# Performance work log

Hardware: AMD Instinct MI355X
Metric: run time of the kernel (lower is better)

## Reference

```python
import jax, jax.numpy as jnp
import numpy as np

B, N_ITEMS, H1, H2 = 1024, 50000, 600, 200


def setup_inputs() -> dict:
    key = jax.random.key(0)
    ks = jax.random.split(key, 8)
    return {
        "x": jax.random.uniform(ks[0], (B, N_ITEMS), dtype=jnp.float32),
        "W1": jax.random.normal(ks[1], (N_ITEMS, H1), dtype=jnp.float32) * 0.02,
        "b1": jax.random.normal(ks[2], (H1,), dtype=jnp.float32) * 0.001,
        "W2": jax.random.normal(ks[3], (H1, H2), dtype=jnp.float32) * 0.05,
        "b2": jax.random.normal(ks[4], (H2,), dtype=jnp.float32) * 0.001,
        "W3": jax.random.normal(ks[5], (H2, H1), dtype=jnp.float32) * 0.05,
        "b3": jax.random.normal(ks[6], (H1,), dtype=jnp.float32) * 0.001,
        "item_emb": jax.random.normal(ks[7], (N_ITEMS, H1), dtype=jnp.float32) * 0.02,
    }


def reference(x, W1, b1, W2, b2, W3, b3, item_emb):
    # F.normalize(input): L2-normalize rows with eps clamp
    norm = jnp.sqrt(jnp.sum(x * x, axis=-1, keepdims=True))
    h = x / jnp.maximum(norm, 1e-12)
    # tanh MLP stack (dropout is identity at inference)
    h = jnp.tanh(h @ W1 + b1)   # [B, 600]
    h = jnp.tanh(h @ W2 + b2)   # [B, 200]
    h = jnp.tanh(h @ W3 + b3)   # [B, 600]
    # pairwise squared-L2 distance to all item embeddings via GEMM decomposition:
    # ||h||^2 - 2 h.e + ||e||^2  (same math as the broadcasted (h-e)^2 sum)
    h_sq = jnp.sum(h * h, axis=-1, keepdims=True)          # [B, 1]
    e_sq = jnp.sum(item_emb * item_emb, axis=-1)           # [N]
    dist = h_sq - 2.0 * (h @ item_emb.T) + e_sq            # [B, N]
    return dist
```

## Files before the change

kernel.cpp:

```cpp
#include <hip/hip_runtime.h>
#include <stdint.h>

namespace {

constexpr int BROWS = 1024;
constexpr int NIT   = 50000;
constexpr int NH1   = 600;
constexpr int NH2   = 200;
constexpr int KXP   = 50016;
constexpr int N1P   = 640;
constexpr int NEP   = 50048;
constexpr int KEP   = 608;
constexpr int KI_TOTAL = KXP / 32;

typedef _Float16 f16x8 __attribute__((ext_vector_type(8)));
typedef _Float16 f16x4 __attribute__((ext_vector_type(4)));
typedef _Float16 f16x2 __attribute__((ext_vector_type(2)));
typedef float    f32x4 __attribute__((ext_vector_type(4)));

__device__ __forceinline__ void gld16(const void* g, void* l) {
  __builtin_amdgcn_global_load_lds(
      (__attribute__((address_space(1))) void*)(void*)g,
      (__attribute__((address_space(3))) void*)l, 16, 0, 0);
}

__global__ __launch_bounds__(256) void norm_conv_k(const float* __restrict__ x,
                                                   float* __restrict__ invnorm,
                                                   _Float16* __restrict__ xh) {
  const int row = blockIdx.x;
  const float4* xr = (const float4*)(x + (size_t)row * NIT);
  float ss = 0.f;
  if (xh != nullptr) {
    f16x4* xo = (f16x4*)(xh + (size_t)row * KXP);
    for (int i = threadIdx.x; i < NIT / 4; i += 256) {
      float4 v = xr[i];
      ss += v.x * v.x + v.y * v.y + v.z * v.z + v.w * v.w;
      f16x4 h;
      h.x = (_Float16)v.x; h.y = (_Float16)v.y;
      h.z = (_Float16)v.z; h.w = (_Float16)v.w;
      xo[i] = h;
    }
    if (threadIdx.x < (KXP - NIT) / 4) {
      f16x4 z;
      z.x = (_Float16)0.f; z.y = (_Float16)0.f;
      z.z = (_Float16)0.f; z.w = (_Float16)0.f;
      xo[NIT / 4 + threadIdx.x] = z;
    }
  } else {
    for (int i = threadIdx.x; i < NIT / 4; i += 256) {
      float4 v = xr[i];
      ss += v.x * v.x + v.y * v.y + v.z * v.z + v.w * v.w;
    }
  }
  for (int o = 32; o > 0; o >>= 1) ss += __shfl_down(ss, o);
  __shared__ float red[4];
  if ((threadIdx.x & 63) == 0) red[threadIdx.x >> 6] = ss;
  __syncthreads();
  if (threadIdx.x == 0) {
    float s = red[0] + red[1] + red[2] + red[3];
    invnorm[row] = 1.0f / fmaxf(sqrtf(s), 1e-12f);
  }
}

__global__ __launch_bounds__(256) void transpose_w1_k(const float* __restrict__ W1,
                                                      _Float16* __restrict__ W1T) {
  __shared__ float tile[64][65];
  const int kb = blockIdx.x * 64;
  const int nb = blockIdx.y * 64;
  const int t = threadIdx.x;
  #pragma unroll
  for (int i = 0; i < 16; ++i) {
    int idx = i * 256 + t;
    int k = idx >> 6, n = idx & 63;
    int gk = kb + k, gn = nb + n;
    tile[k][n] = (gk < NIT && gn < NH1) ? W1[(size_t)gk * NH1 + gn] : 0.f;
  }
  __syncthreads();
  #pragma unroll
  for (int i = 0; i < 8; ++i) {
    int idx = i * 256 + t;
    int n = idx >> 5;
    int k2 = (idx & 31) * 2;
    if (kb + k2 < KXP) {
      f16x2 h;
      h.x = (_Float16)tile[k2][n];
      h.y = (_Float16)tile[k2 + 1][n];
      *(f16x2*)(&W1T[(size_t)(nb + n) * KXP + kb + k2]) = h;
    }
  }
}

__global__ __launch_bounds__(256) void prep_emb_k(const float* __restrict__ emb,
                                                  _Float16* __restrict__ embb,
                                                  float* __restrict__ esq) {
  const int row = blockIdx.x * 4 + (threadIdx.x >> 6);
  const int lane = threadIdx.x & 63;
  const float* er = emb + (size_t)row * NH1;
  float ss = 0.f;
  #pragma unroll
  for (int j = 0; j < 10; ++j) {
    int idx = lane + 64 * j;
    float v = (row < NIT && idx < NH1) ? er[idx] : 0.f;
    ss += v * v;
    if (idx < KEP) embb[(size_t)row * KEP + idx] = (_Float16)v;
  }
  for (int o = 32; o > 0; o >>= 1) ss += __shfl_down(ss, o);
  if (lane == 0) esq[row] = ss;
}

template <int MODE>
__global__ __launch_bounds__(256) void mfma_nt_k(
    const void* __restrict__ Av, const _Float16* __restrict__ Bg,
    float* __restrict__ Cout, const float* __restrict__ hsq,
    const float* __restrict__ esq) {
  __shared__ _Float16 As[128 * 32];
  __shared__ _Float16 Bs[128 * 32];

  const int t = threadIdx.x;
  const int n0 = blockIdx.x * 128;
  const int m0 = blockIdx.y * 128;

  int ki0, ki1, lda, ldb;
  if (MODE == 1) {
    ki0 = 0; ki1 = KEP / 32; lda = KEP; ldb = KEP;
  } else {
    const int Z = (int)gridDim.z;
    const int kiPer = (KI_TOTAL + Z - 1) / Z;
    ki0 = blockIdx.z * kiPer;
    ki1 = ki0 + kiPer;
    if (ki1 > KI_TOTAL) ki1 = KI_TOTAL;
    lda = (MODE == 0) ? NIT : KXP;
    ldb = KXP;
  }

  const int lane = t & 63;
  const int wid = t >> 6;
  const int wm = wid >> 1, wn = wid & 1;
  const int lrow = lane & 15, quad = lane >> 4;

  const f32x4 zero = {0.f, 0.f, 0.f, 0.f};
  f32x4 acc[4][4];
  #pragma unroll
  for (int i = 0; i < 4; ++i)
    #pragma unroll
    for (int j = 0; j < 4; ++j) acc[i][j] = zero;

  for (int ki = ki0; ki < ki1; ++ki) {
    const int k0 = ki * 32;
    if (MODE == 0) {
      const float* A = (const float*)Av;
      #pragma unroll
      for (int j = 0; j < 4; ++j) {
        int g = j * 256 + t;
        int row = g >> 3;
        int kq = (g & 7) * 4;
        float4 v = {0.f, 0.f, 0.f, 0.f};
        if (k0 + kq < NIT)
          v = *(const float4*)(A + (size_t)(m0 + row) * lda + (k0 + kq));
        f16x4 h;
        h.x = (_Float16)v.x; h.y = (_Float16)v.y;
        h.z = (_Float16)v.z; h.w = (_Float16)v.w;
        *(f16x4*)(&As[row * 32 + kq]) = h;
      }
    } else {
      const _Float16* A = (const _Float16*)Av;
      #pragma unroll
      for (int j = 0; j < 2; ++j) {
        int c = j * 256 + t;
        int row = c >> 2, kk = (c & 3) * 8;
        gld16(A + (size_t)(m0 + row) * lda + (k0 + kk), &As[c * 8]);
      }
    }
    #pragma unroll
    for (int j = 0; j < 2; ++j) {
      int c = j * 256 + t;
      int row = c >> 2, kk = (c & 3) * 8;
      gld16(Bg + (size_t)(n0 + row) * ldb + (k0 + kk), &Bs[c * 8]);
    }
    __syncthreads();

    f16x8 af[4], bfr[4];
    #pragma unroll
    for (int mi = 0; mi < 4; ++mi)
      af[mi] = *(const f16x8*)(&As[(wm * 64 + mi * 16 + lrow) * 32 + quad * 8]);
    #pragma unroll
    for (int ni = 0; ni < 4; ++ni)
      bfr[ni] = *(const f16x8*)(&Bs[(wn * 64 + ni * 16 + lrow) * 32 + quad * 8]);
    #pragma unroll
    for (int mi = 0; mi < 4; ++mi)
      #pragma unroll
      for (int ni = 0; ni < 4; ++ni)
        acc[mi][ni] = __builtin_amdgcn_mfma_f32_16x16x32_f16(af[mi], bfr[ni],
                                                             acc[mi][ni], 0, 0, 0);
    __syncthreads();
  }

  if (MODE != 1) {
    float* Cs = Cout + (size_t)blockIdx.z * BROWS * N1P;
    #pragma unroll
    for (int mi = 0; mi < 4; ++mi)
      #pragma unroll
      for (int r = 0; r < 4; ++r) {
        int row = m0 + wm * 64 + mi * 16 + quad * 4 + r;
        #pragma unroll
        for (int ni = 0; ni < 4; ++ni) {
          int col = n0 + wn * 64 + ni * 16 + lrow;
          Cs[(size_t)row * N1P + col] = acc[mi][ni][r];
        }
      }
  } else {
    #pragma unroll
    for (int mi = 0; mi < 4; ++mi)
      #pragma unroll
      for (int r = 0; r < 4; ++r) {
        int row = m0 + wm * 64 + mi * 16 + quad * 4 + r;
        float hv = hsq[row];
        #pragma unroll
        for (int ni = 0; ni < 4; ++ni) {
          int col = n0 + wn * 64 + ni * 16 + lrow;
          if (col < NIT)
            Cout[(size_t)row * NIT + col] = hv - 2.f * acc[mi][ni][r] + esq[col];
        }
      }
  }
}

__global__ __launch_bounds__(256) void reduce_epi1_k(const float* __restrict__ C1p,
                                                     const float* __restrict__ invnorm,
                                                     const float* __restrict__ b1,
                                                     float* __restrict__ h1,
                                                     int nslabs) {
  int idx = blockIdx.x * 256 + threadIdx.x;
  if (idx >= BROWS * NH1) return;
  int m = idx / NH1, n = idx - m * NH1;
  float s = 0.f;
  for (int sp = 0; sp < nslabs; ++sp)
    s += C1p[(size_t)sp * BROWS * N1P + (size_t)m * N1P + n];
  h1[idx] = tanhf(invnorm[m] * s + b1[n]);
}

__global__ __launch_bounds__(256) void gemm2_k(const float* __restrict__ h1,
                                               const float* __restrict__ W2,
                                               const float* __restrict__ b2,
                                               float* __restrict__ h2) {
  __shared__ float hs[8 * NH1];
  const int m0 = blockIdx.x * 8;
  const int t = threadIdx.x;
  for (int i = t; i < 8 * NH1; i += 256) hs[i] = h1[(size_t)m0 * NH1 + i];
  __syncthreads();
  if (t < NH2) {
    float acc[8];
    #pragma unroll
    for (int r = 0; r < 8; ++r) acc[r] = 0.f;
    for (int k = 0; k < NH1; ++k) {
      float w = W2[k * NH2 + t];
      #pragma unroll
      for (int r = 0; r < 8; ++r) acc[r] += hs[r * NH1 + k] * w;
    }
    float bb = b2[t];
    #pragma unroll
    for (int r = 0; r < 8; ++r) h2[(size_t)(m0 + r) * NH2 + t] = tanhf(acc[r] + bb);
  }
}

__global__ __launch_bounds__(256) void gemm3_k(const float* __restrict__ h2,
                                               const float* __restrict__ W3,
                                               const float* __restrict__ b3,
                                               _Float16* __restrict__ h3h,
                                               float* __restrict__ hsq) {
  __shared__ float hs[8 * NH2];
  const int m0 = blockIdx.x * 8;
  const int t = threadIdx.x;
  for (int i = t; i < 8 * NH2; i += 256) hs[i] = h2[(size_t)m0 * NH2 + i];
  __syncthreads();
  float ssq[8];
  #pragma unroll
  for (int r = 0; r < 8; ++r) ssq[r] = 0.f;
  for (int c = 0; c < 3; ++c) {
    int n = t + c * 256;
    if (n < NH1) {
      float acc[8];
      #pragma unroll
      for (int r = 0; r < 8; ++r) acc[r] = 0.f;
      for (int k = 0; k < NH2; ++k) {
        float w = W3[k * NH1 + n];
        #pragma unroll
        for (int r = 0; r < 8; ++r) acc[r] += hs[r * NH2 + k] * w;
      }
      float bb = b3[n];
      #pragma unroll
      for (int r = 0; r < 8; ++r) {
        float v = tanhf(acc[r] + bb);
        h3h[(size_t)(m0 + r) * KEP + n] = (_Float16)v;
        ssq[r] += v * v;
      }
    } else if (n < KEP) {
      #pragma unroll
      for (int r = 0; r < 8; ++r) h3h[(size_t)(m0 + r) * KEP + n] = (_Float16)0.f;
    }
  }
  const int lane = t & 63, wid = t >> 6;
  #pragma unroll
  for (int r = 0; r < 8; ++r)
    for (int o = 32; o > 0; o >>= 1) ssq[r] += __shfl_down(ssq[r], o);
  __shared__ float red2[8][4];
  if (lane == 0) {
    #pragma unroll
    for (int r = 0; r < 8; ++r) red2[r][wid] = ssq[r];
  }
  __syncthreads();
  if (t < 8) hsq[m0 + t] = red2[t][0] + red2[t][1] + red2[t][2] + red2[t][3];
}

}

extern "C" void kernel_launch(void* const* d_in, const int* in_sizes, int n_in,
                              void* d_out, int out_size, void* d_ws, size_t ws_size,
                              hipStream_t stream) {
  const float* x   = (const float*)d_in[0];
  const float* W1  = (const float*)d_in[1];
  const float* b1  = (const float*)d_in[2];
  const float* W2  = (const float*)d_in[3];
  const float* b2  = (const float*)d_in[4];
  const float* W3  = (const float*)d_in[5];
  const float* b3  = (const float*)d_in[6];
  const float* emb = (const float*)d_in[7];
  float* out = (float*)d_out;

  char* ws = (char*)d_ws;

  const size_t XHSZ  = (size_t)BROWS * KXP * 2;
  const size_t W1TSZ = (size_t)N1P * KXP * 2;
  const size_t SLAB  = (size_t)BROWS * N1P * 4;
  const size_t TAIL  = 4096 + 200192 + 2457600 + 819200 + 1245184 + 4096;

  bool useF16A;
  int S;
  const size_t baseA = XHSZ + W1TSZ + TAIL;
  const size_t baseB = W1TSZ + TAIL;
  if (ws_size >= baseA + 16 * SLAB) {
    useF16A = true;
    size_t s = (ws_size - baseA) / SLAB;
    S = s > 32 ? 32 : (int)s;
  } else if (ws_size >= baseB + 8 * SLAB) {
    useF16A = false;
    size_t s = (ws_size - baseB) / SLAB;
    S = s > 32 ? 32 : (int)s;
  } else {
    return;
  }

  size_t off = 0;
  _Float16* xh = nullptr;
  if (useF16A) { xh = (_Float16*)(ws + off); off += XHSZ; }
  const size_t oW1T = off;
  _Float16* W1T = (_Float16*)(ws + off); off += W1TSZ;
  float* C1p = (float*)(ws + off); off += (size_t)S * SLAB;
  float* invn = (float*)(ws + off); off += 4096;
  float* esq  = (float*)(ws + off); off += 200192;
  float* h1   = (float*)(ws + off); off += 2457600;
  float* h2   = (float*)(ws + off); off += 819200;
  _Float16* h3h = (_Float16*)(ws + off); off += 1245184;
  float* hsq  = (float*)(ws + off); off += 4096;
  _Float16* embb = (_Float16*)(ws + oW1T);

  norm_conv_k<<<dim3(BROWS), dim3(256), 0, stream>>>(x, invn, xh);
  transpose_w1_k<<<dim3((KXP + 63) / 64, N1P / 64), dim3(256), 0, stream>>>(W1, W1T);
  if (useF16A) {
    mfma_nt_k<2><<<dim3(N1P / 128, BROWS / 128, S), dim3(256), 0, stream>>>(
        (const void*)xh, W1T, C1p, nullptr, nullptr);
  } else {
    mfma_nt_k<0><<<dim3(N1P / 128, BROWS / 128, S), dim3(256), 0, stream>>>(
        (const void*)x, W1T, C1p, nullptr, nullptr);
  }
  reduce_epi1_k<<<dim3((BROWS * NH1 + 255) / 256), dim3(256), 0, stream>>>(
      C1p, invn, b1, h1, S);
  prep_emb_k<<<dim3(NEP / 4), dim3(256), 0, stream>>>(emb, embb, esq);
  gemm2_k<<<dim3(BROWS / 8), dim3(256), 0, stream>>>(h1, W2, b2, h2);
  gemm3_k<<<dim3(BROWS / 8), dim3(256), 0, stream>>>(h2, W3, b3, h3h, hsq);
  mfma_nt_k<1><<<dim3(NEP / 128, BROWS / 128, 1), dim3(256), 0, stream>>>(
      (const void*)h3h, embb, out, hsq, esq);
}
```

Before: 1.036 ms.

## Double-buffer LDS tiles in MFMA GEMM and unroll the small GEMM loops

The MFMA GEMM kernel now keeps two LDS buffers. It issues the global-to-LDS loads for the next K tile before running the MFMAs on the current one, which hides load latency and needs only one barrier per iteration. An occupancy hint is added to the same kernel. The x row-norm loop is unrolled, and the small W2/W3 GEMMs batch 8 weight loads per step. KXP is padded to a multiple of 64 so the guard in the W1 transpose can be dropped. The cost is double the LDS use per block and larger padded buffers, which must still fit the workspace sizing.

New measurement: 1.010 ms. 1.03x faster.

```diff
diff --git a/kernel.cpp b/kernel.cpp
--- a/kernel.cpp
+++ b/kernel.cpp
@@ -7,7 +7,7 @@
 constexpr int NIT   = 50000;
 constexpr int NH1   = 600;
 constexpr int NH2   = 200;
-constexpr int KXP   = 50016;
+constexpr int KXP   = 50048;
 constexpr int N1P   = 640;
 constexpr int NEP   = 50048;
 constexpr int KEP   = 608;
@@ -32,6 +32,7 @@
   float ss = 0.f;
   if (xh != nullptr) {
     f16x4* xo = (f16x4*)(xh + (size_t)row * KXP);
+    #pragma unroll 4
     for (int i = threadIdx.x; i < NIT / 4; i += 256) {
       float4 v = xr[i];
       ss += v.x * v.x + v.y * v.y + v.z * v.z + v.w * v.w;
@@ -47,6 +48,7 @@
       xo[NIT / 4 + threadIdx.x] = z;
     }
   } else {
+    #pragma unroll 4
     for (int i = threadIdx.x; i < NIT / 4; i += 256) {
       float4 v = xr[i];
       ss += v.x * v.x + v.y * v.y + v.z * v.z + v.w * v.w;
@@ -81,12 +83,10 @@
     int idx = i * 256 + t;
     int n = idx >> 5;
     int k2 = (idx & 31) * 2;
-    if (kb + k2 < KXP) {
-      f16x2 h;
-      h.x = (_Float16)tile[k2][n];
-      h.y = (_Float16)tile[k2 + 1][n];
-      *(f16x2*)(&W1T[(size_t)(nb + n) * KXP + kb + k2]) = h;
-    }
+    f16x2 h;
+    h.x = (_Float16)tile[k2][n];
+    h.y = (_Float16)tile[k2 + 1][n];
+    *(f16x2*)(&W1T[(size_t)(nb + n) * KXP + kb + k2]) = h;
   }
 }
 
@@ -109,12 +109,12 @@
 }
 
 template <int MODE>
-__global__ __launch_bounds__(256) void mfma_nt_k(
+__global__ __launch_bounds__(256, 4) void mfma_nt_k(
     const void* __restrict__ Av, const _Float16* __restrict__ Bg,
     float* __restrict__ Cout, const float* __restrict__ hsq,
     const float* __restrict__ esq) {
-  __shared__ _Float16 As[128 * 32];
-  __shared__ _Float16 Bs[128 * 32];
+  __shared__ _Float16 As[2][128 * 32];
+  __shared__ _Float16 Bs[2][128 * 32];
 
   const int t = threadIdx.x;
   const int n0 = blockIdx.x * 128;
@@ -145,7 +145,7 @@
     #pragma unroll
     for (int j = 0; j < 4; ++j) acc[i][j] = zero;
 
-  for (int ki = ki0; ki < ki1; ++ki) {
+  auto stage = [&](int buf, int ki) {
     const int k0 = ki * 32;
     if (MODE == 0) {
       const float* A = (const float*)Av;
@@ -160,7 +160,7 @@
         f16x4 h;
         h.x = (_Float16)v.x; h.y = (_Float16)v.y;
         h.z = (_Float16)v.z; h.w = (_Float16)v.w;
-        *(f16x4*)(&As[row * 32 + kq]) = h;
+        *(f16x4*)(&As[buf][row * 32 + kq]) = h;
       }
     } else {
       const _Float16* A = (const _Float16*)Av;
@@ -168,24 +168,31 @@
       for (int j = 0; j < 2; ++j) {
         int c = j * 256 + t;
         int row = c >> 2, kk = (c & 3) * 8;
-        gld16(A + (size_t)(m0 + row) * lda + (k0 + kk), &As[c * 8]);
+        gld16(A + (size_t)(m0 + row) * lda + (k0 + kk), &As[buf][c * 8]);
       }
     }
     #pragma unroll
     for (int j = 0; j < 2; ++j) {
       int c = j * 256 + t;
       int row = c >> 2, kk = (c & 3) * 8;
-      gld16(Bg + (size_t)(n0 + row) * ldb + (k0 + kk), &Bs[c * 8]);
-    }
-    __syncthreads();
+      gld16(Bg + (size_t)(n0 + row) * ldb + (k0 + kk), &Bs[buf][c * 8]);
+    }
+  };
+
+  stage(0, ki0);
+  __syncthreads();
+
+  int cur = 0;
+  for (int ki = ki0; ki < ki1; ++ki) {
+    if (ki + 1 < ki1) stage(cur ^ 1, ki + 1);
 
     f16x8 af[4], bfr[4];
     #pragma unroll
     for (int mi = 0; mi < 4; ++mi)
-      af[mi] = *(const f16x8*)(&As[(wm * 64 + mi * 16 + lrow) * 32 + quad * 8]);
+      af[mi] = *(const f16x8*)(&As[cur][(wm * 64 + mi * 16 + lrow) * 32 + quad * 8]);
     #pragma unroll
     for (int ni = 0; ni < 4; ++ni)
-      bfr[ni] = *(const f16x8*)(&Bs[(wn * 64 + ni * 16 + lrow) * 32 + quad * 8]);
+      bfr[ni] = *(const f16x8*)(&Bs[cur][(wn * 64 + ni * 16 + lrow) * 32 + quad * 8]);
     #pragma unroll
     for (int mi = 0; mi < 4; ++mi)
       #pragma unroll
@@ -193,6 +200,7 @@
         acc[mi][ni] = __builtin_amdgcn_mfma_f32_16x16x32_f16(af[mi], bfr[ni],
                                                              acc[mi][ni], 0, 0, 0);
     __syncthreads();
+    cur ^= 1;
   }
 
   if (MODE != 1) {
@@ -252,10 +260,14 @@
     float acc[8];
     #pragma unroll
     for (int r = 0; r < 8; ++r) acc[r] = 0.f;
-    for (int k = 0; k < NH1; ++k) {
-      float w = W2[k * NH2 + t];
-      #pragma unroll
-      for (int r = 0; r < 8; ++r) acc[r] += hs[r * NH1 + k] * w;
+    for (int k0 = 0; k0 < NH1; k0 += 8) {
+      float w[8];
+      #pragma unroll
+      for (int u = 0; u < 8; ++u) w[u] = W2[(k0 + u) * NH2 + t];
+      #pragma unroll
+      for (int u = 0; u < 8; ++u)
+        #pragma unroll
+        for (int r = 0; r < 8; ++r) acc[r] += hs[r * NH1 + k0 + u] * w[u];
     }
     float bb = b2[t];
     #pragma unroll
@@ -282,10 +294,14 @@
       float acc[8];
       #pragma unroll
       for (int r = 0; r < 8; ++r) acc[r] = 0.f;
-      for (int k = 0; k < NH2; ++k) {
-        float w = W3[k * NH1 + n];
-        #pragma unroll
-        for (int r = 0; r < 8; ++r) acc[r] += hs[r * NH2 + k] * w;
+      for (int k0 = 0; k0 < NH2; k0 += 8) {
+        float w[8];
+        #pragma unroll
+        for (int u = 0; u < 8; ++u) w[u] = W3[(k0 + u) * NH1 + n];
+        #pragma unroll
+        for (int u = 0; u < 8; ++u)
+          #pragma unroll
+          for (int r = 0; r < 8; ++r) acc[r] += hs[r * NH2 + k0 + u] * w[u];
       }
       float bb = b3[n];
       #pragma unroll
@@ -365,7 +381,7 @@
   _Float16* embb = (_Float16*)(ws + oW1T);
 
   norm_conv_k<<<dim3(BROWS), dim3(256), 0, stream>>>(x, invn, xh);
-  transpose_w1_k<<<dim3((KXP + 63) / 64, N1P / 64), dim3(256), 0, stream>>>(W1, W1T);
+  transpose_w1_k<<<dim3(KXP / 64, N1P / 64), dim3(256), 0, stream>>>(W1, W1T);
   if (useF16A) {
     mfma_nt_k<2><<<dim3(N1P / 128, BROWS / 128, S), dim3(256), 0, stream>>>(
         (const void*)xh, W1T, C1p, nullptr, nullptr);
```
